# Optimization experiments

Hardware: AMD Instinct MI355X
Metric: run time of the kernel (lower is better)

The kernel has to match this reference:

```python
import math
import jax, jax.numpy as jnp
import numpy as np

FACTOR = 5


def setup_inputs() -> dict:
    key = jax.random.key(0)
    kq, kk, kv, ki = jax.random.split(key, 4)
    B, H, L, D = 4, 8, 2048, 64
    sample_k = min(FACTOR * math.ceil(math.log(L)), L)  # 40
    queries = jax.random.normal(kq, (B, H, L, D), dtype=jnp.float32)
    keys = jax.random.normal(kk, (B, H, L, D), dtype=jnp.float32)
    values = jax.random.normal(kv, (B, H, L, D), dtype=jnp.float32)
    index_sample = jax.random.randint(ki, (L, sample_k), 0, L, dtype=jnp.int64 if jax.config.jax_enable_x64 else jnp.int32)
    return {"queries": queries, "keys": keys, "values": values, "index_sample": index_sample}


def reference(queries, keys, values, index_sample):
    B, H, L_Q, D = queries.shape
    L_K = keys.shape[2]
    u = min(FACTOR * math.ceil(math.log(L_Q)), L_Q)  # n_top queries (= 40)
    scale = 1.0 / math.sqrt(D)

    # --- _prob_QK: sparsity measurement over randomly sampled keys ---
    # K_sample[b,h,q,s,:] = keys[b,h,index_sample[q,s],:]  -> [B,H,L_Q,S,D]
    K_sample = keys[:, :, index_sample, :]
    Q_K_sample = jnp.einsum('bhqd,bhqsd->bhqs', queries, K_sample)  # [B,H,L_Q,S]
    M = Q_K_sample.max(axis=-1) - Q_K_sample.sum(axis=-1) / L_K      # [B,H,L_Q]
    _, M_top = jax.lax.top_k(M, u)                                    # [B,H,u]

    Q_reduce = jnp.take_along_axis(queries, M_top[..., None], axis=2)  # [B,H,u,D]
    scores_top = jnp.einsum('bhud,bhkd->bhuk', Q_reduce, keys) * scale  # [B,H,u,L_K]

    # --- initial context: causal cumulative sum of V (mask_flag=True) ---
    context = jnp.cumsum(values, axis=2)  # [B,H,L_Q,D]

    # --- ProbMask: causal rows gathered at the selected query indices ---
    causal = jnp.triu(jnp.ones((L_Q, L_K), dtype=bool), 1)  # [L_Q,L_K]
    mask = causal[M_top]                                     # [B,H,u,L_K]
    scores_top = jnp.where(mask, -jnp.inf, scores_top)

    attn = jax.nn.softmax(scores_top, axis=-1)                       # [B,H,u,L_K]
    update = jnp.einsum('bhuk,bhkd->bhud', attn, values)             # [B,H,u,D]

    b_idx = jnp.arange(B)[:, None, None]
    h_idx = jnp.arange(H)[None, :, None]
    context = context.at[b_idx, h_idx, M_top].set(update.astype(context.dtype))
    return context
```

## Files before the change

kernel.cpp:

```cpp
#include <hip/hip_runtime.h>
#include <math.h>

#define BB 4
#define HH 8
#define LL 2048
#define DD 64
#define SK 40
#define BH (BB*HH)
#define NC 16
#define CK 128

__device__ __forceinline__ unsigned ordu(float v) {
    unsigned u = __float_as_uint(v);
    return (u & 0x80000000u) ? ~u : (u | 0x80000000u);
}

__device__ __forceinline__ float dot4(float4 a, float4 b) {
    return a.x * b.x + a.y * b.y + a.z * b.z + a.w * b.w;
}

__global__ __launch_bounds__(256) void stage1_kernel(
        const float* __restrict__ Q, const float* __restrict__ K,
        const float* __restrict__ V, const int* __restrict__ IDX,
        float* __restrict__ M, float* __restrict__ csum) {
    int tid = threadIdx.x;
    int b = blockIdx.x;
    int bhLo = b & 7;
    int bhA = bhLo + 8 * ((b >> 3) & 1);
    int bhB = bhA + 16;
    int chunk = b >> 4;
    int qbase = chunk * 64;
    int w = tid >> 6, lane = tid & 63;
    int qw = lane >> 2, c = lane & 3;
    int qi = w * 16 + qw;
    int qpos = qbase + qi;

    __shared__ int sidx[64 * SK];
    __shared__ float part[4][DD];

    for (int i = tid; i < 64 * SK; i += 256) sidx[i] = IDX[(size_t)qbase * SK + i];

    const float4* Q4 = (const float4*)Q;
    const float4* K4 = (const float4*)K;
    float4 qA[4], qB[4];
    #pragma unroll
    for (int j = 0; j < 4; ++j) {
        qA[j] = Q4[((size_t)bhA * LL + qpos) * 16 + j * 4 + c];
        qB[j] = Q4[((size_t)bhB * LL + qpos) * 16 + j * 4 + c];
    }
    __syncthreads();

    size_t kbA = (size_t)bhA * LL * 16;
    size_t kbB = (size_t)bhB * LL * 16;
    float mxA = -INFINITY, smA = 0.f, mxB = -INFINITY, smB = 0.f;

    float4 a0[4], b0[4], a1[4], b1[4];
    {
        int ks = sidx[qi * SK];
        const float4* krA = K4 + kbA + (size_t)ks * 16;
        const float4* krB = K4 + kbB + (size_t)ks * 16;
        #pragma unroll
        for (int j = 0; j < 4; ++j) { a0[j] = krA[j * 4 + c]; b0[j] = krB[j * 4 + c]; }
    }
    for (int s = 0; s < SK; s += 2) {
        {
            int ks = sidx[qi * SK + s + 1];
            const float4* krA = K4 + kbA + (size_t)ks * 16;
            const float4* krB = K4 + kbB + (size_t)ks * 16;
            #pragma unroll
            for (int j = 0; j < 4; ++j) { a1[j] = krA[j * 4 + c]; b1[j] = krB[j * 4 + c]; }
        }
        {
            float pA = dot4(qA[0], a0[0]) + dot4(qA[1], a0[1])
                     + dot4(qA[2], a0[2]) + dot4(qA[3], a0[3]);
            float pB = dot4(qB[0], b0[0]) + dot4(qB[1], b0[1])
                     + dot4(qB[2], b0[2]) + dot4(qB[3], b0[3]);
            pA += __shfl_xor(pA, 1, 64); pA += __shfl_xor(pA, 2, 64);
            pB += __shfl_xor(pB, 1, 64); pB += __shfl_xor(pB, 2, 64);
            mxA = fmaxf(mxA, pA); smA += pA;
            mxB = fmaxf(mxB, pB); smB += pB;
        }
        if (s + 2 < SK) {
            int ks = sidx[qi * SK + s + 2];
            const float4* krA = K4 + kbA + (size_t)ks * 16;
            const float4* krB = K4 + kbB + (size_t)ks * 16;
            #pragma unroll
            for (int j = 0; j < 4; ++j) { a0[j] = krA[j * 4 + c]; b0[j] = krB[j * 4 + c]; }
        }
        {
            float pA = dot4(qA[0], a1[0]) + dot4(qA[1], a1[1])
                     + dot4(qA[2], a1[2]) + dot4(qA[3], a1[3]);
            float pB = dot4(qB[0], b1[0]) + dot4(qB[1], b1[1])
                     + dot4(qB[2], b1[2]) + dot4(qB[3], b1[3]);
            pA += __shfl_xor(pA, 1, 64); pA += __shfl_xor(pA, 2, 64);
            pB += __shfl_xor(pB, 1, 64); pB += __shfl_xor(pB, 2, 64);
            mxA = fmaxf(mxA, pA); smA += pA;
            mxB = fmaxf(mxB, pB); smB += pB;
        }
    }
    if (c == 0) {
        M[(size_t)bhA * LL + qpos] = mxA - smA * (1.0f / (float)LL);
        M[(size_t)bhB * LL + qpos] = mxB - smB * (1.0f / (float)LL);
    }

    {
        int bhv = (b & 7) + 8 * ((b >> 3) & 3);
        int cv = b >> 5;
        int d = tid & 63, sg = tid >> 6;
        size_t base = (size_t)bhv * LL * DD;
        int row0 = cv * 128 + sg * 32;
        float s2 = 0.f;
        for (int j = 0; j < 32; ++j) s2 += V[base + (size_t)(row0 + j) * DD + d];
        part[sg][d] = s2;
        __syncthreads();
        if (sg == 0)
            csum[((size_t)bhv * 16 + cv) * DD + d] =
                part[0][d] + part[1][d] + part[2][d] + part[3][d];
    }
}

__global__ __launch_bounds__(256) void radix_kernel(
        const float* __restrict__ M, int* __restrict__ topk) {
    int tid = threadIdx.x;
    int bh = blockIdx.x;
    __shared__ unsigned hist[256];
    __shared__ unsigned sfx[256];
    __shared__ unsigned bc_prefix, bc_need;
    __shared__ unsigned cnt_gt, cnt_eq;
    __shared__ int eqlist[128];

    unsigned v[8];
    #pragma unroll
    for (int j = 0; j < 8; ++j)
        v[j] = ordu(M[(size_t)bh * LL + tid + j * 256]);

    unsigned prefix = 0, need = SK;
    #pragma unroll
    for (int pass = 0; pass < 4; ++pass) {
        const int s = 24 - 8 * pass;
        const unsigned maskHigh = (pass == 0) ? 0u : (0xFFFFFFFFu << (s + 8));
        hist[tid] = 0;
        __syncthreads();
        #pragma unroll
        for (int j = 0; j < 8; ++j)
            if (((v[j] ^ prefix) & maskHigh) == 0)
                atomicAdd(&hist[(v[j] >> s) & 0xFF], 1u);
        __syncthreads();
        sfx[tid] = hist[tid];
        __syncthreads();
        #pragma unroll
        for (int off = 1; off < 256; off <<= 1) {
            unsigned t = (tid + off < 256) ? sfx[tid + off] : 0u;
            __syncthreads();
            sfx[tid] += t;
            __syncthreads();
        }
        unsigned above = (tid < 255) ? sfx[tid + 1] : 0u;
        if (above < need && sfx[tid] >= need) {
            bc_prefix = prefix | ((unsigned)tid << s);
            bc_need = need - above;
        }
        __syncthreads();
        prefix = bc_prefix;
        need = bc_need;
        __syncthreads();
    }
    unsigned T = prefix;
    if (tid == 0) { cnt_gt = 0; cnt_eq = 0; }
    __syncthreads();
    #pragma unroll
    for (int j = 0; j < 8; ++j) {
        int idx = tid + j * 256;
        if (v[j] > T) { unsigned p = atomicAdd(&cnt_gt, 1u); topk[bh * SK + p] = idx; }
        else if (v[j] == T) { unsigned p = atomicAdd(&cnt_eq, 1u); if (p < 128) eqlist[p] = idx; }
    }
    __syncthreads();
    if (tid == 0) {
        int ne = (int)min(cnt_eq, 128u);
        unsigned base = cnt_gt;
        for (unsigned r2 = 0; r2 < need; ++r2) {
            int bj = 0, bv = 0x7FFFFFFF;
            for (int j = 0; j < ne; ++j)
                if (eqlist[j] < bv) { bv = eqlist[j]; bj = j; }
            topk[bh * SK + base + r2] = bv;
            eqlist[bj] = 0x7FFFFFFF;
        }
    }
}

__global__ __launch_bounds__(256) void attn_cumsum_kernel(
        const float* __restrict__ Q, const float* __restrict__ K,
        const float* __restrict__ V, const int* __restrict__ topk,
        const float* __restrict__ csum, float* __restrict__ out,
        float* __restrict__ pm, float* __restrict__ pl,
        float* __restrict__ po) {
    int tid = threadIdx.x;
    __shared__ int qp[SK];
    __shared__ float4 sq4[SK][16];
    __shared__ float SC[CK][SK + 1];
    __shared__ float part[4][DD];

    if (blockIdx.x < 512) {
        int x = blockIdx.x;
        int bhLo = x & 7;
        int r = x >> 3;
        int c = r & 15;
        int bhHi = r >> 4;
        int bh = bhHi * 8 + bhLo;
        int w = tid >> 6, lane = tid & 63;
        int cbase = c * CK;

        if (tid < SK) qp[tid] = topk[bh * SK + tid];
        __syncthreads();
        const float4* Q4 = (const float4*)Q;
        const float4* K4 = (const float4*)K;
        const float4* V4 = (const float4*)V;
        for (int i = tid; i < SK * 16; i += 256) {
            int u = i >> 4, j = i & 15;
            sq4[u][j] = Q4[((size_t)bh * LL + qp[u]) * 16 + j];
        }
        __syncthreads();

        {
            int half = tid & 1;
            int kk = tid >> 1;
            int kg = cbase + kk;
            size_t kb4 = (size_t)bh * LL * 16;
            float4 kreg[8];
            const float4* kr = K4 + kb4 + (size_t)kg * 16 + half * 8;
            #pragma unroll
            for (int j = 0; j < 8; ++j) kreg[j] = kr[j];
            #pragma unroll 4
            for (int u = 0; u < SK; ++u) {
                int qpu = qp[u];
                if (cbase > qpu) {
                    if (half == 0) SC[kk][u] = -INFINITY;
                    continue;
                }
                float pa = 0.f, pb = 0.f;
                #pragma unroll
                for (int j = 0; j < 4; ++j) {
                    float4 qv = sq4[u][half * 8 + j];
                    pa += kreg[j].x * qv.x + kreg[j].y * qv.y + kreg[j].z * qv.z + kreg[j].w * qv.w;
                }
                #pragma unroll
                for (int j = 4; j < 8; ++j) {
                    float4 qv = sq4[u][half * 8 + j];
                    pb += kreg[j].x * qv.x + kreg[j].y * qv.y + kreg[j].z * qv.z + kreg[j].w * qv.w;
                }
                float p = pa + pb;
                p += __shfl_xor(p, 1, 64);
                if (half == 0) SC[kk][u] = (kg <= qpu) ? p * 0.125f : -INFINITY;
            }
        }
        __syncthreads();

        for (int u = w; u < SK; u += 4) {
            float s0 = SC[lane][u], s1 = SC[lane + 64][u];
            float m = fmaxf(s0, s1);
            #pragma unroll
            for (int off = 32; off > 0; off >>= 1) m = fmaxf(m, __shfl_xor(m, off, 64));
            float e0 = 0.f, e1 = 0.f;
            if (m != -INFINITY) {
                e0 = expf(s0 - m);
                e1 = expf(s1 - m);
            }
            SC[lane][u] = e0;
            SC[lane + 64][u] = e1;
            float ls = e0 + e1;
            #pragma unroll
            for (int off = 32; off > 0; off >>= 1) ls += __shfl_xor(ls, off, 64);
            if (lane == 0) {
                size_t pb = (size_t)(bh * SK + u) * NC + c;
                pm[pb] = m;
                pl[pb] = ls;
            }
        }
        __syncthreads();

        {
            int ks = tid & 3;
            int dg = (tid >> 2) & 15;
            int ug = tid >> 6;
            int u0 = ug * 10;
            float4 acc[10];
            #pragma unroll
            for (int i = 0; i < 10; ++i) acc[i] = make_float4(0.f, 0.f, 0.f, 0.f);
            for (int t = 0; t < CK / 4; ++t) {
                int k = t * 4 + ks;
                float4 vv = V4[((size_t)bh * LL + cbase + k) * 16 + dg];
                #pragma unroll
                for (int i = 0; i < 10; ++i) {
                    float pw = SC[k][u0 + i];
                    acc[i].x += pw * vv.x; acc[i].y += pw * vv.y;
                    acc[i].z += pw * vv.z; acc[i].w += pw * vv.w;
                }
            }
            #pragma unroll
            for (int i = 0; i < 10; ++i) {
                acc[i].x += __shfl_xor(acc[i].x, 1, 64); acc[i].x += __shfl_xor(acc[i].x, 2, 64);
                acc[i].y += __shfl_xor(acc[i].y, 1, 64); acc[i].y += __shfl_xor(acc[i].y, 2, 64);
                acc[i].z += __shfl_xor(acc[i].z, 1, 64); acc[i].z += __shfl_xor(acc[i].z, 2, 64);
                acc[i].w += __shfl_xor(acc[i].w, 1, 64); acc[i].w += __shfl_xor(acc[i].w, 2, 64);
            }
            if (ks == 0) {
                #pragma unroll
                for (int i = 0; i < 10; ++i) {
                    float4* dst = (float4*)&po[((size_t)(bh * SK + u0 + i) * NC + c) * DD + dg * 4];
                    *dst = acc[i];
                }
            }
        }
    } else {
        int x = blockIdx.x - 512;
        int bhLo = x & 7, r = x >> 3;
        int bhHi = r & 3, c = r >> 2;
        int bh = bhHi * 8 + bhLo;
        int d = tid & 63, sg = tid >> 6;
        size_t base = (size_t)bh * LL * DD;
        int row0 = c * 128 + sg * 32;
        float v[32];
        #pragma unroll
        for (int j = 0; j < 32; ++j) v[j] = V[base + (size_t)(row0 + j) * DD + d];
        float s = 0.f;
        #pragma unroll
        for (int j = 0; j < 32; ++j) s += v[j];
        part[sg][d] = s;
        __syncthreads();
        float pre = 0.f;
        for (int cc = 0; cc < c; ++cc) pre += csum[((size_t)bh * 16 + cc) * DD + d];
        for (int ss = 0; ss < sg; ++ss) pre += part[ss][d];
        float acc = pre;
        #pragma unroll
        for (int j = 0; j < 32; ++j) {
            acc += v[j];
            out[base + (size_t)(row0 + j) * DD + d] = acc;
        }
    }
}

__global__ __launch_bounds__(256) void combine_kernel(
        const float* __restrict__ pm, const float* __restrict__ pl,
        const float* __restrict__ po, const int* __restrict__ topk,
        float* __restrict__ out) {
    int g = blockIdx.x * 4 + (threadIdx.x >> 6);
    int d = threadIdx.x & 63;
    int qpos = topk[g];
    int bh = g / SK;
    size_t gb = (size_t)g * NC;
    float gm = -INFINITY;
    #pragma unroll
    for (int j = 0; j < NC; ++j) gm = fmaxf(gm, pm[gb + j]);
    float L = 0.f, o = 0.f;
    #pragma unroll
    for (int j = 0; j < NC; ++j) {
        float pmj = pm[gb + j];
        float wj = (pmj == -INFINITY) ? 0.f : expf(pmj - gm);
        L += pl[gb + j] * wj;
        o += po[(gb + j) * DD + d] * wj;
    }
    out[((size_t)bh * LL + qpos) * DD + d] = o / L;
}

extern "C" void kernel_launch(void* const* d_in, const int* in_sizes, int n_in,
                              void* d_out, int out_size, void* d_ws, size_t ws_size,
                              hipStream_t stream) {
    const float* Q   = (const float*)d_in[0];
    const float* K   = (const float*)d_in[1];
    const float* V   = (const float*)d_in[2];
    const int*   IDX = (const int*)d_in[3];
    float* out = (float*)d_out;

    char* ws = (char*)d_ws;
    float* M    = (float*)ws;  ws += (size_t)BH * LL * sizeof(float);
    int*   topk = (int*)ws;    ws += ((size_t)BH * SK * sizeof(int) + 255) & ~255ull;
    float* csum = (float*)ws;  ws += (size_t)BH * 16 * DD * sizeof(float);
    float* pm   = (float*)ws;  ws += ((size_t)BH * SK * NC * sizeof(float) + 255) & ~255ull;
    float* pl   = (float*)ws;  ws += ((size_t)BH * SK * NC * sizeof(float) + 255) & ~255ull;
    float* po   = (float*)ws;

    stage1_kernel<<<512, 256, 0, stream>>>(Q, K, V, IDX, M, csum);
    radix_kernel<<<32, 256, 0, stream>>>(M, topk);
    attn_cumsum_kernel<<<1024, 256, 0, stream>>>(Q, K, V, topk, csum, out, pm, pl, po);
    combine_kernel<<<320, 256, 0, stream>>>(pm, pl, po, topk, out);
}
```

Measured before the change: 154.1 us.

## Double attention key chunk size and transpose score tile for vectorized access

Attention blocks now process 256-key chunks (8 chunks per head) instead of 128, so each thread holds two key rows and reuses each Q load from shared memory for both. The score tile is transposed to [query][key] with padding, which lets the softmax and the PV accumulation read float4 vectors, and the PV loop now consumes four V rows per step. Fewer partial chunks shrink the combine work. The trade-off is that attention blocks drop from 512 to 256, and register pressure rises under the new launch bound of 3.

```diff
diff --git a/kernel.cpp b/kernel.cpp
--- a/kernel.cpp
+++ b/kernel.cpp
@@ -7,8 +7,9 @@
 #define DD 64
 #define SK 40
 #define BH (BB*HH)
-#define NC 16
-#define CK 128
+#define NC 8
+#define CK 256
+#define SCP (CK + 4)
 
 __device__ __forceinline__ unsigned ordu(float v) {
     unsigned u = __float_as_uint(v);
@@ -188,7 +189,7 @@
     }
 }
 
-__global__ __launch_bounds__(256) void attn_cumsum_kernel(
+__global__ __launch_bounds__(256, 3) void attn_cumsum_kernel(
         const float* __restrict__ Q, const float* __restrict__ K,
         const float* __restrict__ V, const int* __restrict__ topk,
         const float* __restrict__ csum, float* __restrict__ out,
@@ -197,15 +198,15 @@
     int tid = threadIdx.x;
     __shared__ int qp[SK];
     __shared__ float4 sq4[SK][16];
-    __shared__ float SC[CK][SK + 1];
+    __shared__ float SCT[SK][SCP];
     __shared__ float part[4][DD];
 
-    if (blockIdx.x < 512) {
+    if (blockIdx.x < 256) {
         int x = blockIdx.x;
         int bhLo = x & 7;
         int r = x >> 3;
-        int c = r & 15;
-        int bhHi = r >> 4;
+        int c = r & 7;
+        int bhHi = r >> 3;
         int bh = bhHi * 8 + bhLo;
         int w = tid >> 6, lane = tid & 63;
         int cbase = c * CK;
@@ -224,50 +225,51 @@
         {
             int half = tid & 1;
             int kk = tid >> 1;
-            int kg = cbase + kk;
+            int kg1 = cbase + kk;
+            int kg2 = cbase + kk + 128;
             size_t kb4 = (size_t)bh * LL * 16;
-            float4 kreg[8];
-            const float4* kr = K4 + kb4 + (size_t)kg * 16 + half * 8;
-            #pragma unroll
-            for (int j = 0; j < 8; ++j) kreg[j] = kr[j];
+            float4 k1[8], k2[8];
+            const float4* kr1 = K4 + kb4 + (size_t)kg1 * 16 + half * 8;
+            const float4* kr2 = K4 + kb4 + (size_t)kg2 * 16 + half * 8;
+            #pragma unroll
+            for (int j = 0; j < 8; ++j) { k1[j] = kr1[j]; k2[j] = kr2[j]; }
             #pragma unroll 4
             for (int u = 0; u < SK; ++u) {
                 int qpu = qp[u];
                 if (cbase > qpu) {
-                    if (half == 0) SC[kk][u] = -INFINITY;
+                    if (half == 0) { SCT[u][kk] = -INFINITY; SCT[u][kk + 128] = -INFINITY; }
                     continue;
                 }
-                float pa = 0.f, pb = 0.f;
+                float p1 = 0.f, p2 = 0.f;
                 #pragma unroll
-                for (int j = 0; j < 4; ++j) {
+                for (int j = 0; j < 8; ++j) {
                     float4 qv = sq4[u][half * 8 + j];
-                    pa += kreg[j].x * qv.x + kreg[j].y * qv.y + kreg[j].z * qv.z + kreg[j].w * qv.w;
-                }
-                #pragma unroll
-                for (int j = 4; j < 8; ++j) {
-                    float4 qv = sq4[u][half * 8 + j];
-                    pb += kreg[j].x * qv.x + kreg[j].y * qv.y + kreg[j].z * qv.z + kreg[j].w * qv.w;
-                }
-                float p = pa + pb;
-                p += __shfl_xor(p, 1, 64);
-                if (half == 0) SC[kk][u] = (kg <= qpu) ? p * 0.125f : -INFINITY;
-            }
-        }
-        __syncthreads();
-
-        for (int u = w; u < SK; u += 4) {
-            float s0 = SC[lane][u], s1 = SC[lane + 64][u];
-            float m = fmaxf(s0, s1);
+                    p1 += dot4(k1[j], qv);
+                    p2 += dot4(k2[j], qv);
+                }
+                p1 += __shfl_xor(p1, 1, 64);
+                p2 += __shfl_xor(p2, 1, 64);
+                if (half == 0) {
+                    SCT[u][kk]       = (kg1 <= qpu) ? p1 * 0.125f : -INFINITY;
+                    SCT[u][kk + 128] = (kg2 <= qpu) ? p2 * 0.125f : -INFINITY;
+                }
+            }
+        }
+        __syncthreads();
+
+        for (int ui = 0; ui < 10; ++ui) {
+            int u = w * 10 + ui;
+            float4 sv = *(const float4*)&SCT[u][lane * 4];
+            float m = fmaxf(fmaxf(sv.x, sv.y), fmaxf(sv.z, sv.w));
             #pragma unroll
             for (int off = 32; off > 0; off >>= 1) m = fmaxf(m, __shfl_xor(m, off, 64));
-            float e0 = 0.f, e1 = 0.f;
+            float4 ev = make_float4(0.f, 0.f, 0.f, 0.f);
             if (m != -INFINITY) {
-                e0 = expf(s0 - m);
-                e1 = expf(s1 - m);
-            }
-            SC[lane][u] = e0;
-            SC[lane + 64][u] = e1;
-            float ls = e0 + e1;
+                ev.x = expf(sv.x - m); ev.y = expf(sv.y - m);
+                ev.z = expf(sv.z - m); ev.w = expf(sv.w - m);
+            }
+            *(float4*)&SCT[u][lane * 4] = ev;
+            float ls = ev.x + ev.y + ev.z + ev.w;
             #pragma unroll
             for (int off = 32; off > 0; off >>= 1) ls += __shfl_xor(ls, off, 64);
             if (lane == 0) {
@@ -286,14 +288,19 @@
             float4 acc[10];
             #pragma unroll
             for (int i = 0; i < 10; ++i) acc[i] = make_float4(0.f, 0.f, 0.f, 0.f);
-            for (int t = 0; t < CK / 4; ++t) {
-                int k = t * 4 + ks;
-                float4 vv = V4[((size_t)bh * LL + cbase + k) * 16 + dg];
+            for (int t = 0; t < CK / 16; ++t) {
+                int k0 = t * 16 + ks * 4;
+                float4 vv0 = V4[((size_t)bh * LL + cbase + k0 + 0) * 16 + dg];
+                float4 vv1 = V4[((size_t)bh * LL + cbase + k0 + 1) * 16 + dg];
+                float4 vv2 = V4[((size_t)bh * LL + cbase + k0 + 2) * 16 + dg];
+                float4 vv3 = V4[((size_t)bh * LL + cbase + k0 + 3) * 16 + dg];
                 #pragma unroll
                 for (int i = 0; i < 10; ++i) {
-                    float pw = SC[k][u0 + i];
-                    acc[i].x += pw * vv.x; acc[i].y += pw * vv.y;
-                    acc[i].z += pw * vv.z; acc[i].w += pw * vv.w;
+                    float4 pw = *(const float4*)&SCT[u0 + i][k0];
+                    acc[i].x += pw.x * vv0.x + pw.y * vv1.x + pw.z * vv2.x + pw.w * vv3.x;
+                    acc[i].y += pw.x * vv0.y + pw.y * vv1.y + pw.z * vv2.y + pw.w * vv3.y;
+                    acc[i].z += pw.x * vv0.z + pw.y * vv1.z + pw.z * vv2.z + pw.w * vv3.z;
+                    acc[i].w += pw.x * vv0.w + pw.y * vv1.w + pw.z * vv2.w + pw.w * vv3.w;
                 }
             }
             #pragma unroll
@@ -312,7 +319,7 @@
             }
         }
     } else {
-        int x = blockIdx.x - 512;
+        int x = blockIdx.x - 256;
         int bhLo = x & 7, r = x >> 3;
         int bhHi = r & 3, c = r >> 2;
         int bh = bhHi * 8 + bhLo;
@@ -381,6 +388,6 @@
 
     stage1_kernel<<<512, 256, 0, stream>>>(Q, K, V, IDX, M, csum);
     radix_kernel<<<32, 256, 0, stream>>>(M, topk);
-    attn_cumsum_kernel<<<1024, 256, 0, stream>>>(Q, K, V, topk, csum, out, pm, pl, po);
+    attn_cumsum_kernel<<<768, 256, 0, stream>>>(Q, K, V, topk, csum, out, pm, pl, po);
     combine_kernel<<<320, 256, 0, stream>>>(pm, pl, po, topk, out);
 }
```

Measured after the change: 158.5 us. 1.03x slower.
